# Kernel optimization log

Hardware: AMD Instinct MI355X
Metric: run time of the kernel (lower is better)

Reference implementation:

```python
import jax, jax.numpy as jnp
import numpy as np

B, N, C, H = 8, 4096, 384, 8
HD = C // H  # 48
KERNEL_EPS = 1e-3
EPS = 1e-8


def setup_inputs() -> dict:
    key = jax.random.key(0)
    k1, k2, k3, k4 = jax.random.split(key, 4)
    x = jax.random.normal(k1, (B, N, C), dtype=jnp.float32)
    Wqkv = jax.random.normal(k2, (3 * C, C), dtype=jnp.float32) * 0.02
    Wproj = jax.random.normal(k3, (C, C), dtype=jnp.float32) * 0.02
    bproj = jax.random.normal(k4, (C,), dtype=jnp.float32) * 0.02
    return {"x": x, "Wqkv": Wqkv, "Wproj": Wproj, "bproj": bproj}


def reference(x, Wqkv, Wproj, bproj):
    # qkv projection (no bias): (B,N,3C) -> (3,B,H,N,HD)
    qkv = jnp.einsum('bnc,dc->bnd', x, Wqkv).reshape(B, N, 3, H, HD)
    qkv = jnp.transpose(qkv, (2, 0, 3, 1, 4))
    q, k, v = qkv[0], qkv[1], qkv[2]

    # generalized_kernel with projection_matrix=None, kernel_fn=ReLU
    dn = HD ** (-0.25)  # data normalizer
    qp = jax.nn.relu(dn * q) + KERNEL_EPS  # (B,H,N,HD) feature map, m=HD
    kp = jax.nn.relu(dn * k) + KERNEL_EPS

    ks = kp.sum(axis=2)                              # (B,H,m)
    D = jnp.einsum('bhnm,bhm->bhn', qp, ks)          # (B,H,N)
    kptv = jnp.einsum('bhnd,bhnm->bhdm', v, kp)      # (B,H,HD,m)
    out = jnp.einsum('bhnm,bhdm->bhnd', qp, kptv) / (D[..., None] + EPS)

    # faithful to original: reshape (B,H,N,HD) -> (B,N,C) WITHOUT head transpose
    out = out.reshape(B, N, C)
    return jnp.einsum('bnc,dc->bnd', out, Wproj) + bproj
```

## Files before the change

### kernel.cpp

```cpp
#include <hip/hip_runtime.h>
#include <hip/hip_bf16.h>


typedef __attribute__((ext_vector_type(8))) short short8;
typedef __attribute__((ext_vector_type(4))) float floatx4;

#define MFMA(a, b, c) __builtin_amdgcn_mfma_f32_16x16x32_bf16((a), (b), (c), 0, 0, 0)

__device__ __forceinline__ unsigned short f2bf(float f) {
  union { float f; unsigned u; } x; x.f = f;
  unsigned r = x.u + 0x7FFFu + ((x.u >> 16) & 1u);
  return (unsigned short)(r >> 16);
}

__device__ __forceinline__ void cv4(const float* __restrict__ in, unsigned short* __restrict__ out, int i) {
  float4 v = *(const float4*)(in + i);
  uint2 o;
  o.x = (unsigned)f2bf(v.x) | ((unsigned)f2bf(v.y) << 16);
  o.y = (unsigned)f2bf(v.z) | ((unsigned)f2bf(v.w) << 16);
  *(uint2*)(out + i) = o;
}

__global__ void conv_w(const float* __restrict__ wq, const float* __restrict__ wp,
                       unsigned short* __restrict__ wqb, unsigned short* __restrict__ wpb,
                       float* __restrict__ accD) {
  const int tid = blockIdx.x * blockDim.x + threadIdx.x;
  const int stride = gridDim.x * blockDim.x * 4;
  for (int i = tid * 4; i < 442368; i += stride) cv4(wq, wqb, i);
  for (int i = tid * 4; i < 147456; i += stride) cv4(wp, wpb, i);
  float4 z = {0.f, 0.f, 0.f, 0.f};
  for (int i = tid * 4; i < 196608; i += stride) *(float4*)(accD + i) = z;
}

__global__ __launch_bounds__(256, 2) void gemm_qkv(
    const float* __restrict__ x,
    const unsigned short* __restrict__ Wq,
    unsigned short* __restrict__ qp,
    float* __restrict__ accD) {
  __shared__ unsigned short As[128 * 64];
  __shared__ unsigned short Bs[128 * 64];
  __shared__ unsigned short Tt[2][48 * 136];

  const int cpx = gridDim.x >> 3;
  const int bid = (blockIdx.x & 7) * cpx + (blockIdx.x >> 3);
  const int mt = bid / 11;
  const int j = bid - mt * 11;
  const int tid = threadIdx.x;
  const int w = tid >> 6, lane = tid & 63;
  const int wm = w >> 1, wn = w & 1;
  const int l15 = lane & 15, l4 = lane >> 4;
  const int isQ = (j < 3);
  const int h = j - 3;

  floatx4 zero = {0.f, 0.f, 0.f, 0.f};
  floatx4 acc[4][4];
#pragma unroll
  for (int i = 0; i < 4; ++i)
#pragma unroll
    for (int jj = 0; jj < 4; ++jj) acc[i][jj] = zero;

  const size_t Abase = (size_t)mt * 128 * 384;
  const int arow = tid >> 4;
  const int akf = (tid & 15) * 4;

  float4 xv[8];
#pragma unroll
  for (int p = 0; p < 8; ++p)
    xv[p] = *(const float4*)&x[Abase + (size_t)(p * 16 + arow) * 384 + akf];

  for (int k0 = 0; k0 < 384; k0 += 64) {
    if (isQ) {
      const size_t Bb = (size_t)(j * 128) * 384;
#pragma unroll
      for (int i = 0; i < 4; ++i) {
        int li = w * 256 + i * 64 + lane;
        int row = li >> 3, col = (li & 7) << 3;
        __builtin_amdgcn_global_load_lds(
            (const __attribute__((address_space(1))) void*)(Wq + Bb + (size_t)row * 384 + k0 + col),
            (__attribute__((address_space(3))) void*)&Bs[row * 64 + col], 16, 0, 0);
      }
    } else {
#pragma unroll
      for (int i = 0; i < 3; ++i) {
        int idx = i * 256 + tid;
        int row = idx >> 3, col = (idx & 7) << 3;
        int srow = (row < 48) ? (384 + h * 48 + row) : (720 + h * 48 + row);
        __builtin_amdgcn_global_load_lds(
            (const __attribute__((address_space(1))) void*)(Wq + (size_t)srow * 384 + k0 + col),
            (__attribute__((address_space(3))) void*)&Bs[row * 64 + col], 16, 0, 0);
      }
    }
#pragma unroll
    for (int p = 0; p < 8; ++p) {
      int row = p * 16 + arow;
      uint2 o;
      o.x = (unsigned)f2bf(xv[p].x) | ((unsigned)f2bf(xv[p].y) << 16);
      o.y = (unsigned)f2bf(xv[p].z) | ((unsigned)f2bf(xv[p].w) << 16);
      *(uint2*)&As[row * 64 + akf] = o;
    }
    __syncthreads();
    if (k0 < 320) {
#pragma unroll
      for (int p = 0; p < 8; ++p)
        xv[p] = *(const float4*)&x[Abase + (size_t)(p * 16 + arow) * 384 + k0 + 64 + akf];
    }
#pragma unroll
    for (int kk = 0; kk < 2; ++kk) {
      short8 a[4];
#pragma unroll
      for (int mf = 0; mf < 4; ++mf)
        a[mf] = *(const short8*)&As[(wm * 64 + mf * 16 + l15) * 64 + kk * 32 + l4 * 8];
      if (isQ) {
#pragma unroll
        for (int nf = 0; nf < 4; ++nf) {
          short8 b = *(const short8*)&Bs[(wn * 64 + nf * 16 + l15) * 64 + kk * 32 + l4 * 8];
#pragma unroll
          for (int mf = 0; mf < 4; ++mf) acc[mf][nf] = MFMA(a[mf], b, acc[mf][nf]);
        }
      } else {
#pragma unroll
        for (int nf = 0; nf < 3; ++nf) {
          short8 b = *(const short8*)&Bs[(wn * 48 + nf * 16 + l15) * 64 + kk * 32 + l4 * 8];
#pragma unroll
          for (int mf = 0; mf < 4; ++mf) acc[mf][nf] = MFMA(a[mf], b, acc[mf][nf]);
        }
      }
    }
    __syncthreads();
  }

  const float DN = 0.3799178430f;
  if (isQ) {
#pragma unroll
    for (int mf = 0; mf < 4; ++mf) {
#pragma unroll
      for (int nf = 0; nf < 4; ++nf) {
        int gm0 = mt * 128 + wm * 64 + mf * 16 + l4 * 4;
        int gn = j * 128 + wn * 64 + nf * 16 + l15;
#pragma unroll
        for (int r = 0; r < 4; ++r) {
          float v = fmaxf(acc[mf][nf][r] * DN, 0.f) + 1e-3f;
          qp[(size_t)(gm0 + r) * 384 + gn] = f2bf(v);
        }
      }
    }
  } else {
#pragma unroll
    for (int nf = 0; nf < 3; ++nf) {
#pragma unroll
      for (int mf = 0; mf < 4; ++mf) {
        float v0 = acc[mf][nf][0], v1 = acc[mf][nf][1];
        float v2 = acc[mf][nf][2], v3 = acc[mf][nf][3];
        if (wn == 0) {
          v0 = fmaxf(v0 * DN, 0.f) + 1e-3f;
          v1 = fmaxf(v1 * DN, 0.f) + 1e-3f;
          v2 = fmaxf(v2 * DN, 0.f) + 1e-3f;
          v3 = fmaxf(v3 * DN, 0.f) + 1e-3f;
        }
        uint2 o;
        o.x = (unsigned)f2bf(v0) | ((unsigned)f2bf(v1) << 16);
        o.y = (unsigned)f2bf(v2) | ((unsigned)f2bf(v3) << 16);
        *(uint2*)&Tt[wn][(nf * 16 + l15) * 136 + wm * 64 + mf * 16 + l4 * 4] = o;
      }
    }
    __syncthreads();
    short8 ones;
    {
      unsigned short ov = (l15 == 0) ? (unsigned short)0x3F80 : (unsigned short)0;
#pragma unroll
      for (int e = 0; e < 8; ++e) ones[e] = (short)ov;
    }
    floatx4 acc2[3];
#pragma unroll
    for (int i = 0; i < 3; ++i) acc2[i] = zero;
#pragma unroll
    for (int c = 0; c < 4; ++c) {
      short8 af;
      if (w < 3)
        af = *(const short8*)&Tt[1][(w * 16 + l15) * 136 + c * 32 + l4 * 8];
      else
        af = ones;
#pragma unroll
      for (int mfr = 0; mfr < 3; ++mfr) {
        short8 bf8 = *(const short8*)&Tt[0][(mfr * 16 + l15) * 136 + c * 32 + l4 * 8];
        acc2[mfr] = MFMA(af, bf8, acc2[mfr]);
      }
    }
    float* dst = accD + (size_t)((mt >> 5) * 8 + h) * 3072;
    if (w < 3) {
#pragma unroll
      for (int mfr = 0; mfr < 3; ++mfr)
#pragma unroll
        for (int r = 0; r < 4; ++r)
          atomicAdd(&dst[(w * 16 + l4 * 4 + r) * 48 + mfr * 16 + l15], acc2[mfr][r]);
    } else if (l4 == 0) {
#pragma unroll
      for (int mfr = 0; mfr < 3; ++mfr)
        atomicAdd(&dst[48 * 48 + mfr * 16 + l15], acc2[mfr][0]);
    }
  }
}

__global__ __launch_bounds__(256, 2) void attn_out(
    const unsigned short* __restrict__ qp,
    const float* __restrict__ accD,
    unsigned short* __restrict__ outr) {
  __shared__ unsigned short Qs[256 * 52 + 64];
  const int bh = blockIdx.x >> 4, tg = blockIdx.x & 15;
  const int b = bh >> 3, h = bh & 7;
  const int tid = threadIdx.x, w = tid >> 6, lane = tid & 63;
  const int l15 = lane & 15, l4 = lane >> 4;
  const int t0 = tg * 256 + w * 64;
  const size_t rb = (size_t)b * 4096;

  short8 bfr[2][4];
#pragma unroll
  for (int kk = 0; kk < 2; ++kk) {
#pragma unroll
    for (int nf = 0; nf < 4; ++nf) {
      int row = nf * 16 + l15;
      int c0 = kk * 32 + l4 * 8;
      short8 f;
      if (kk == 1 && l4 >= 2) {
#pragma unroll
        for (int e = 0; e < 8; ++e) f[e] = 0;
      } else {
        const float* p = accD + (size_t)bh * 3072 + row * 48 + c0;
        float4 v0 = *(const float4*)p;
        float4 v1 = *(const float4*)(p + 4);
        f[0] = (short)f2bf(v0.x); f[1] = (short)f2bf(v0.y);
        f[2] = (short)f2bf(v0.z); f[3] = (short)f2bf(v0.w);
        f[4] = (short)f2bf(v1.x); f[5] = (short)f2bf(v1.y);
        f[6] = (short)f2bf(v1.z); f[7] = (short)f2bf(v1.w);
      }
      bfr[kk][nf] = f;
    }
  }

#pragma unroll
  for (int c = 0; c < 6; ++c) {
    int idx = c * 256 + tid;
    int row = idx / 6;
    int part = idx - row * 6;
    short8 v = *(const short8*)&qp[(rb + tg * 256 + row) * 384 + h * 48 + part * 8];
    *(short8*)&Qs[row * 52 + part * 8] = v;
  }
  *(uint2*)&Qs[tid * 52 + 48] = (uint2){0u, 0u};
  if (tid < 64) Qs[256 * 52 + tid] = 0;
  __syncthreads();

  floatx4 zero = {0.f, 0.f, 0.f, 0.f};
  floatx4 acc[4][4];
#pragma unroll
  for (int i = 0; i < 4; ++i)
#pragma unroll
    for (int j = 0; j < 4; ++j) acc[i][j] = zero;

#pragma unroll
  for (int mf = 0; mf < 4; ++mf) {
#pragma unroll
    for (int kk = 0; kk < 2; ++kk) {
      short8 a = *(const short8*)&Qs[(w * 64 + mf * 16 + l15) * 52 + kk * 32 + l4 * 8];
#pragma unroll
      for (int nf = 0; nf < 4; ++nf)
        acc[mf][nf] = MFMA(a, bfr[kk][nf], acc[mf][nf]);
    }
  }

#pragma unroll
  for (int mf = 0; mf < 4; ++mf) {
    float inv[4];
#pragma unroll
    for (int r = 0; r < 4; ++r) {
      float den = __shfl(acc[mf][3][r], lane & 48, 64) + 1e-8f;
      inv[r] = __builtin_amdgcn_rcpf(den);
    }
#pragma unroll
    for (int nf = 0; nf < 3; ++nf) {
#pragma unroll
      for (int r = 0; r < 4; ++r) {
        int tt = t0 + mf * 16 + l4 * 4 + r;
        int d = nf * 16 + l15;
        float v = acc[mf][nf][r] * inv[r];
        int np = h * 512 + (tt >> 3);
        int cp = (tt & 7) * 48 + d;
        outr[(rb + np) * 384 + cp] = f2bf(v);
      }
    }
  }
}

__global__ __launch_bounds__(256, 2) void gemm_proj(
    const unsigned short* __restrict__ A,
    const unsigned short* __restrict__ Bt,
    float* __restrict__ Cout,
    const float* __restrict__ bias) {
  __shared__ unsigned short As[128 * 64];
  __shared__ unsigned short Bs[128 * 64];
  const int NT = 3;
  const int cpx = gridDim.x >> 3;
  const int bid = (blockIdx.x & 7) * cpx + (blockIdx.x >> 3);
  const int bn = bid % NT;
  const int bm = bid / NT;
  const int tid = threadIdx.x;
  const int w = tid >> 6, lane = tid & 63;
  const int wm = w >> 1, wn = w & 1;
  const int l15 = lane & 15, l4 = lane >> 4;

  floatx4 zero = {0.f, 0.f, 0.f, 0.f};
  floatx4 acc[4][4];
#pragma unroll
  for (int i = 0; i < 4; ++i)
#pragma unroll
    for (int j = 0; j < 4; ++j) acc[i][j] = zero;

  const int li0 = (w * 4) * 64 + lane;
  const size_t Abase = (size_t)(bm * 128) * 384;
  const size_t Bbase = (size_t)(bn * 128) * 384;

  for (int k0 = 0; k0 < 384; k0 += 64) {
#pragma unroll
    for (int i = 0; i < 4; ++i) {
      int li = li0 + i * 64;
      int row = li >> 3;
      int col = (li & 7) << 3;
      __builtin_amdgcn_global_load_lds(
          (const __attribute__((address_space(1))) void*)(A + Abase + (size_t)row * 384 + k0 + col),
          (__attribute__((address_space(3))) void*)&As[(w * 4 + i) * 512], 16, 0, 0);
      __builtin_amdgcn_global_load_lds(
          (const __attribute__((address_space(1))) void*)(Bt + Bbase + (size_t)row * 384 + k0 + col),
          (__attribute__((address_space(3))) void*)&Bs[(w * 4 + i) * 512], 16, 0, 0);
    }
    __syncthreads();
#pragma unroll
    for (int kk = 0; kk < 2; ++kk) {
      short8 a[4], b[4];
#pragma unroll
      for (int mf = 0; mf < 4; ++mf)
        a[mf] = *(const short8*)&As[(wm * 64 + mf * 16 + l15) * 64 + kk * 32 + l4 * 8];
#pragma unroll
      for (int nf = 0; nf < 4; ++nf)
        b[nf] = *(const short8*)&Bs[(wn * 64 + nf * 16 + l15) * 64 + kk * 32 + l4 * 8];
#pragma unroll
      for (int mf = 0; mf < 4; ++mf)
#pragma unroll
        for (int nf = 0; nf < 4; ++nf)
          acc[mf][nf] = MFMA(a[mf], b[nf], acc[mf][nf]);
    }
    __syncthreads();
  }

#pragma unroll
  for (int mf = 0; mf < 4; ++mf) {
#pragma unroll
    for (int nf = 0; nf < 4; ++nf) {
      int gm0 = bm * 128 + wm * 64 + mf * 16 + l4 * 4;
      int gn = bn * 128 + wn * 64 + nf * 16 + l15;
#pragma unroll
      for (int r = 0; r < 4; ++r)
        Cout[(size_t)(gm0 + r) * 384 + gn] = acc[mf][nf][r] + bias[gn];
    }
  }
}

extern "C" void kernel_launch(void* const* d_in, const int* in_sizes, int n_in,
                              void* d_out, int out_size, void* d_ws, size_t ws_size,
                              hipStream_t stream) {
  const float* x = (const float*)d_in[0];
  const float* Wqkv = (const float*)d_in[1];
  const float* Wproj = (const float*)d_in[2];
  const float* bproj = (const float*)d_in[3];

  char* ws = (char*)d_ws;
  unsigned short* qp = (unsigned short*)(ws);
  float* accD = (float*)(ws + 25165824);
  unsigned short* outr = (unsigned short*)(ws + 25952256);
  unsigned short* wqkvb = (unsigned short*)(ws + 51118080);
  unsigned short* wprojb = (unsigned short*)(ws + 52002816);

  conv_w<<<256, 256, 0, stream>>>(Wqkv, Wproj, wqkvb, wprojb, accD);
  gemm_qkv<<<2816, 256, 0, stream>>>(x, wqkvb, qp, accD);
  attn_out<<<1024, 256, 0, stream>>>(qp, accD, outr);
  gemm_proj<<<768, 256, 0, stream>>>(outr, wprojb, (float*)d_out, bproj);
}
```

Before: 195.8 us.

## Fuse attention output with projection GEMM and alias shared memory buffers

Merges attn_out and gemm_proj into one kernel. Each block computes a 256-token slice of one head, which maps to 32 output rows after the head-mixing reshape, stages those rows as bf16 in shared memory and multiplies them by a 128-column slice of Wproj. This removes the bf16 intermediate round trip through global memory and one launch. The cost is that each attention slice is recomputed once per column tile (three times), and the projection tile per block shrinks to 32x128. Shared buffers are unioned in both kernels so occupancy can rise to 3 blocks per SM.

New measurement: 310.1 us. +58.4%, slower.

```diff
diff --git a/kernel.cpp b/kernel.cpp
--- a/kernel.cpp
+++ b/kernel.cpp
@@ -32,14 +32,16 @@
   for (int i = tid * 4; i < 196608; i += stride) *(float4*)(accD + i) = z;
 }
 
-__global__ __launch_bounds__(256, 2) void gemm_qkv(
+__global__ __launch_bounds__(256, 3) void gemm_qkv(
     const float* __restrict__ x,
     const unsigned short* __restrict__ Wq,
     unsigned short* __restrict__ qp,
     float* __restrict__ accD) {
-  __shared__ unsigned short As[128 * 64];
+  __shared__ union {
+    unsigned short As[128 * 64];
+    unsigned short Tt[2][48 * 136];
+  } ua;
   __shared__ unsigned short Bs[128 * 64];
-  __shared__ unsigned short Tt[2][48 * 136];
 
   const int cpx = gridDim.x >> 3;
   const int bid = (blockIdx.x & 7) * cpx + (blockIdx.x >> 3);
@@ -96,7 +98,7 @@
       uint2 o;
       o.x = (unsigned)f2bf(xv[p].x) | ((unsigned)f2bf(xv[p].y) << 16);
       o.y = (unsigned)f2bf(xv[p].z) | ((unsigned)f2bf(xv[p].w) << 16);
-      *(uint2*)&As[row * 64 + akf] = o;
+      *(uint2*)&ua.As[row * 64 + akf] = o;
     }
     __syncthreads();
     if (k0 < 320) {
@@ -109,7 +111,7 @@
       short8 a[4];
 #pragma unroll
       for (int mf = 0; mf < 4; ++mf)
-        a[mf] = *(const short8*)&As[(wm * 64 + mf * 16 + l15) * 64 + kk * 32 + l4 * 8];
+        a[mf] = *(const short8*)&ua.As[(wm * 64 + mf * 16 + l15) * 64 + kk * 32 + l4 * 8];
       if (isQ) {
 #pragma unroll
         for (int nf = 0; nf < 4; ++nf) {
@@ -160,7 +162,7 @@
         uint2 o;
         o.x = (unsigned)f2bf(v0) | ((unsigned)f2bf(v1) << 16);
         o.y = (unsigned)f2bf(v2) | ((unsigned)f2bf(v3) << 16);
-        *(uint2*)&Tt[wn][(nf * 16 + l15) * 136 + wm * 64 + mf * 16 + l4 * 4] = o;
+        *(uint2*)&ua.Tt[wn][(nf * 16 + l15) * 136 + wm * 64 + mf * 16 + l4 * 4] = o;
       }
     }
     __syncthreads();
@@ -177,12 +179,12 @@
     for (int c = 0; c < 4; ++c) {
       short8 af;
       if (w < 3)
-        af = *(const short8*)&Tt[1][(w * 16 + l15) * 136 + c * 32 + l4 * 8];
+        af = *(const short8*)&ua.Tt[1][(w * 16 + l15) * 136 + c * 32 + l4 * 8];
       else
         af = ones;
 #pragma unroll
       for (int mfr = 0; mfr < 3; ++mfr) {
-        short8 bf8 = *(const short8*)&Tt[0][(mfr * 16 + l15) * 136 + c * 32 + l4 * 8];
+        short8 bf8 = *(const short8*)&ua.Tt[0][(mfr * 16 + l15) * 136 + c * 32 + l4 * 8];
         acc2[mfr] = MFMA(af, bf8, acc2[mfr]);
       }
     }
@@ -201,16 +203,28 @@
   }
 }
 
-__global__ __launch_bounds__(256, 2) void attn_out(
+__global__ __launch_bounds__(256, 3) void attn_proj(
     const unsigned short* __restrict__ qp,
     const float* __restrict__ accD,
-    unsigned short* __restrict__ outr) {
-  __shared__ unsigned short Qs[256 * 52 + 64];
-  const int bh = blockIdx.x >> 4, tg = blockIdx.x & 15;
-  const int b = bh >> 3, h = bh & 7;
+    const unsigned short* __restrict__ Wp,
+    const float* __restrict__ bias,
+    float* __restrict__ Cout) {
+  __shared__ union {
+    unsigned short Qs[256 * 52 + 64];
+    unsigned short Af[32 * 392];
+  } uq;
+  __shared__ unsigned short Bs[128 * 64];
+
+  const int cpx = gridDim.x >> 3;
+  const int bid = (blockIdx.x & 7) * cpx + (blockIdx.x >> 3);
+  const int bm = bid / 3;
+  const int bn = bid - bm * 3;
+  const int b = bm >> 7;
+  const int h = (bm >> 4) & 7;
+  const int n0 = (bm & 15) * 256;
+  const int bh = b * 8 + h;
   const int tid = threadIdx.x, w = tid >> 6, lane = tid & 63;
   const int l15 = lane & 15, l4 = lane >> 4;
-  const int t0 = tg * 256 + w * 64;
   const size_t rb = (size_t)b * 4096;
 
   short8 bfr[2][4];
@@ -242,11 +256,11 @@
     int idx = c * 256 + tid;
     int row = idx / 6;
     int part = idx - row * 6;
-    short8 v = *(const short8*)&qp[(rb + tg * 256 + row) * 384 + h * 48 + part * 8];
-    *(short8*)&Qs[row * 52 + part * 8] = v;
-  }
-  *(uint2*)&Qs[tid * 52 + 48] = (uint2){0u, 0u};
-  if (tid < 64) Qs[256 * 52 + tid] = 0;
+    short8 v = *(const short8*)&qp[(rb + n0 + row) * 384 + h * 48 + part * 8];
+    *(short8*)&uq.Qs[row * 52 + part * 8] = v;
+  }
+  *(uint2*)&uq.Qs[tid * 52 + 48] = (uint2){0u, 0u};
+  if (tid < 64) uq.Qs[256 * 52 + tid] = 0;
   __syncthreads();
 
   floatx4 zero = {0.f, 0.f, 0.f, 0.f};
@@ -260,12 +274,13 @@
   for (int mf = 0; mf < 4; ++mf) {
 #pragma unroll
     for (int kk = 0; kk < 2; ++kk) {
-      short8 a = *(const short8*)&Qs[(w * 64 + mf * 16 + l15) * 52 + kk * 32 + l4 * 8];
+      short8 a = *(const short8*)&uq.Qs[(w * 64 + mf * 16 + l15) * 52 + kk * 32 + l4 * 8];
 #pragma unroll
       for (int nf = 0; nf < 4; ++nf)
         acc[mf][nf] = MFMA(a, bfr[kk][nf], acc[mf][nf]);
     }
   }
+  __syncthreads();
 
 #pragma unroll
   for (int mf = 0; mf < 4; ++mf) {
@@ -279,86 +294,56 @@
     for (int nf = 0; nf < 3; ++nf) {
 #pragma unroll
       for (int r = 0; r < 4; ++r) {
-        int tt = t0 + mf * 16 + l4 * 4 + r;
+        int t = w * 64 + mf * 16 + l4 * 4 + r;
         int d = nf * 16 + l15;
-        float v = acc[mf][nf][r] * inv[r];
-        int np = h * 512 + (tt >> 3);
-        int cp = (tt & 7) * 48 + d;
-        outr[(rb + np) * 384 + cp] = f2bf(v);
-      }
-    }
-  }
-}
-
-__global__ __launch_bounds__(256, 2) void gemm_proj(
-    const unsigned short* __restrict__ A,
-    const unsigned short* __restrict__ Bt,
-    float* __restrict__ Cout,
-    const float* __restrict__ bias) {
-  __shared__ unsigned short As[128 * 64];
-  __shared__ unsigned short Bs[128 * 64];
-  const int NT = 3;
-  const int cpx = gridDim.x >> 3;
-  const int bid = (blockIdx.x & 7) * cpx + (blockIdx.x >> 3);
-  const int bn = bid % NT;
-  const int bm = bid / NT;
-  const int tid = threadIdx.x;
-  const int w = tid >> 6, lane = tid & 63;
-  const int wm = w >> 1, wn = w & 1;
-  const int l15 = lane & 15, l4 = lane >> 4;
-
-  floatx4 zero = {0.f, 0.f, 0.f, 0.f};
-  floatx4 acc[4][4];
-#pragma unroll
-  for (int i = 0; i < 4; ++i)
-#pragma unroll
-    for (int j = 0; j < 4; ++j) acc[i][j] = zero;
-
-  const int li0 = (w * 4) * 64 + lane;
-  const size_t Abase = (size_t)(bm * 128) * 384;
-  const size_t Bbase = (size_t)(bn * 128) * 384;
+        uq.Af[(t >> 3) * 392 + (t & 7) * 48 + d] = f2bf(acc[mf][nf][r] * inv[r]);
+      }
+    }
+  }
+
+  floatx4 accp[2][2];
+#pragma unroll
+  for (int i = 0; i < 2; ++i)
+#pragma unroll
+    for (int j = 0; j < 2; ++j) accp[i][j] = zero;
 
   for (int k0 = 0; k0 < 384; k0 += 64) {
 #pragma unroll
     for (int i = 0; i < 4; ++i) {
-      int li = li0 + i * 64;
-      int row = li >> 3;
-      int col = (li & 7) << 3;
+      int idx = i * 256 + tid;
+      int row = idx >> 3, col = (idx & 7) << 3;
       __builtin_amdgcn_global_load_lds(
-          (const __attribute__((address_space(1))) void*)(A + Abase + (size_t)row * 384 + k0 + col),
-          (__attribute__((address_space(3))) void*)&As[(w * 4 + i) * 512], 16, 0, 0);
-      __builtin_amdgcn_global_load_lds(
-          (const __attribute__((address_space(1))) void*)(Bt + Bbase + (size_t)row * 384 + k0 + col),
-          (__attribute__((address_space(3))) void*)&Bs[(w * 4 + i) * 512], 16, 0, 0);
+          (const __attribute__((address_space(1))) void*)(Wp + (size_t)(bn * 128 + row) * 384 + k0 + col),
+          (__attribute__((address_space(3))) void*)&Bs[row * 64 + col], 16, 0, 0);
     }
     __syncthreads();
 #pragma unroll
     for (int kk = 0; kk < 2; ++kk) {
-      short8 a[4], b[4];
-#pragma unroll
-      for (int mf = 0; mf < 4; ++mf)
-        a[mf] = *(const short8*)&As[(wm * 64 + mf * 16 + l15) * 64 + kk * 32 + l4 * 8];
-#pragma unroll
-      for (int nf = 0; nf < 4; ++nf)
-        b[nf] = *(const short8*)&Bs[(wn * 64 + nf * 16 + l15) * 64 + kk * 32 + l4 * 8];
-#pragma unroll
-      for (int mf = 0; mf < 4; ++mf)
-#pragma unroll
-        for (int nf = 0; nf < 4; ++nf)
-          acc[mf][nf] = MFMA(a[mf], b[nf], acc[mf][nf]);
-    }
-    __syncthreads();
-  }
-
-#pragma unroll
-  for (int mf = 0; mf < 4; ++mf) {
-#pragma unroll
-    for (int nf = 0; nf < 4; ++nf) {
-      int gm0 = bm * 128 + wm * 64 + mf * 16 + l4 * 4;
-      int gn = bn * 128 + wn * 64 + nf * 16 + l15;
+      short8 a[2], bfp[2];
+#pragma unroll
+      for (int mf = 0; mf < 2; ++mf)
+        a[mf] = *(const short8*)&uq.Af[(mf * 16 + l15) * 392 + k0 + kk * 32 + l4 * 8];
+#pragma unroll
+      for (int nf = 0; nf < 2; ++nf)
+        bfp[nf] = *(const short8*)&Bs[(w * 32 + nf * 16 + l15) * 64 + kk * 32 + l4 * 8];
+#pragma unroll
+      for (int mf = 0; mf < 2; ++mf)
+#pragma unroll
+        for (int nf = 0; nf < 2; ++nf)
+          accp[mf][nf] = MFMA(a[mf], bfp[nf], accp[mf][nf]);
+    }
+    __syncthreads();
+  }
+
+#pragma unroll
+  for (int mf = 0; mf < 2; ++mf) {
+#pragma unroll
+    for (int nf = 0; nf < 2; ++nf) {
+      int gm0 = bm * 32 + mf * 16 + l4 * 4;
+      int gn = bn * 128 + w * 32 + nf * 16 + l15;
 #pragma unroll
       for (int r = 0; r < 4; ++r)
-        Cout[(size_t)(gm0 + r) * 384 + gn] = acc[mf][nf][r] + bias[gn];
+        Cout[(size_t)(gm0 + r) * 384 + gn] = accp[mf][nf][r] + bias[gn];
     }
   }
 }
@@ -374,12 +359,10 @@
   char* ws = (char*)d_ws;
   unsigned short* qp = (unsigned short*)(ws);
   float* accD = (float*)(ws + 25165824);
-  unsigned short* outr = (unsigned short*)(ws + 25952256);
-  unsigned short* wqkvb = (unsigned short*)(ws + 51118080);
-  unsigned short* wprojb = (unsigned short*)(ws + 52002816);
+  unsigned short* wqkvb = (unsigned short*)(ws + 25952256);
+  unsigned short* wprojb = (unsigned short*)(ws + 26836992);
 
   conv_w<<<256, 256, 0, stream>>>(Wqkv, Wproj, wqkvb, wprojb, accD);
   gemm_qkv<<<2816, 256, 0, stream>>>(x, wqkvb, qp, accD);
-  attn_out<<<1024, 256, 0, stream>>>(qp, accD, outr);
-  gemm_proj<<<768, 256, 0, stream>>>(outr, wprojb, (float*)d_out, bproj);
-}
+  attn_proj<<<3072, 256, 0, stream>>>(qp, accD, wprojb, bproj, (float*)d_out);
+}
```
